# Performance work log

Measured on AMD Instinct MI355X. Metric: run time of the kernel, lower is better.

## Reference

```python
import jax, jax.numpy as jnp
import numpy as np

N, R, E, DIN, DOUT, B = 40000, 16, 50000, 256, 256, 4


def setup_inputs() -> dict:
    key = jax.random.key(0)
    ks = jax.random.split(key, 7)
    xav = (2.0 / (DIN + DOUT)) ** 0.5  # xavier-ish scale
    x = jax.random.normal(ks[0], (N, DIN), jnp.float32)
    bases = jax.random.normal(ks[1], (B, DIN, DOUT), jnp.float32) * xav
    coeff = jax.random.normal(ks[2], (R, B), jnp.float32) * 0.5
    loop_weight = jax.random.normal(ks[3], (DIN, DOUT), jnp.float32) * xav
    h_bias = jnp.zeros((DOUT,), jnp.float32)
    edge_src = jax.random.randint(ks[4], (R, E), 0, N, dtype=jnp.int64)
    edge_dst = jax.random.randint(ks[5], (R, E), 0, N, dtype=jnp.int64)
    return {"x": x, "bases": bases, "coeff": coeff, "loop_weight": loop_weight,
            "h_bias": h_bias, "edge_src": edge_src, "edge_dst": edge_dst}


def reference(x, bases, coeff, loop_weight, h_bias, edge_src, edge_dst):
    # Basis decomposition: per-relation weight W_r = sum_b coeff[r,b] * bases[b]
    W = jnp.einsum('rb,bio->rio', coeff, bases)  # [R, DIN, DOUT]
    n = x.shape[0]

    def body(acc, rel):
        W_r, src, dst = rel
        # transform all nodes once, gather at edge sources
        m = (x @ W_r)[src]                                   # [E, DOUT]
        agg = jax.ops.segment_sum(m, dst, num_segments=n)    # [N, DOUT]
        deg = jax.ops.segment_sum(jnp.ones(src.shape, jnp.float32), dst,
                                  num_segments=n)            # in-degree per rel
        # norm='right': divide by dst in-degree (clamped to 1)
        return acc + agg / jnp.clip(deg, 1.0)[:, None], None

    h0 = jnp.zeros((n, loop_weight.shape[1]), x.dtype)
    h, _ = jax.lax.scan(body, h0, (W, edge_src, edge_dst))   # sum over relations
    h = h + x @ loop_weight + h_bias                         # self-loop + bias
    return jax.nn.relu(h)
```

## Files before the change

kernel.cpp:

```cpp
#include <hip/hip_runtime.h>

#define NN   40000
#define RR   16
#define EE   50000
#define DD   256
#define NB   4
#define KTOT (NB*DD + DD)

#define SCAN_BLK  40
#define SCAN_ELEM 1024

typedef __bf16 bf16x8 __attribute__((ext_vector_type(8)));
typedef float  f32x4  __attribute__((ext_vector_type(4)));
typedef float  f32x2  __attribute__((ext_vector_type(2)));
typedef unsigned short ushort_t;

__device__ inline unsigned short f2bf(float f) {
    unsigned int b = __builtin_bit_cast(unsigned int, f);
    b += 0x7FFFu + ((b >> 16) & 1u);
    return (unsigned short)(b >> 16);
}


__global__ __launch_bounds__(256) void k_cast(const float* __restrict__ x,
                                              const float* __restrict__ bases,
                                              const float* __restrict__ lw,
                                              ushort_t* __restrict__ xb,
                                              ushort_t* __restrict__ Bt) {
    int t = blockIdx.x * blockDim.x + threadIdx.x;
    const int NX = NN * DD / 4;
    if (t < NX) {
        float4 f = *(const float4*)(x + (size_t)t * 4);
        ushort4 o;
        o.x = f2bf(f.x); o.y = f2bf(f.y); o.z = f2bf(f.z); o.w = f2bf(f.w);
        *(ushort4*)(xb + (size_t)t * 4) = o;
    } else {
        int u = t - NX;
        if (u < DD * KTOT) {
            int o = u / KTOT, k = u - o * KTOT;
            float f = (k < NB * DD) ? bases[(size_t)k * DD + o]
                                    : lw[(size_t)(k - NB * DD) * DD + o];
            Bt[u] = f2bf(f);
        }
    }
}

__global__ __launch_bounds__(256) void k_deg(const int* __restrict__ edst,
                                             int* __restrict__ deg) {
    int e = blockIdx.x * blockDim.x + threadIdx.x;
    if (e >= RR * EE) return;
    int r = e / EE;
    atomicAdd(&deg[r * NN + edst[e]], 1);
}

__global__ __launch_bounds__(256) void k_hist(const int* __restrict__ deg,
                                              int* __restrict__ hist) {
    int i = blockIdx.x * blockDim.x + threadIdx.x;
    if (i >= NN) return;
    int s = 0;
#pragma unroll
    for (int r = 0; r < RR; r++) s += deg[r * NN + i];
    hist[i] = s;
}

__global__ __launch_bounds__(256) void k_scanA(const int* __restrict__ hist,
                                               int* __restrict__ offsets,
                                               int* __restrict__ bsum) {
    __shared__ int part[256];
    int t = threadIdx.x, b = blockIdx.x;
    int g = b * SCAN_ELEM + t * 4;
    int4 h = {0, 0, 0, 0};
    if (g + 3 < NN) h = *(const int4*)(hist + g);
    else {
        if (g + 0 < NN) h.x = hist[g + 0];
        if (g + 1 < NN) h.y = hist[g + 1];
        if (g + 2 < NN) h.z = hist[g + 2];
        if (g + 3 < NN) h.w = hist[g + 3];
    }
    int s = h.x + h.y + h.z + h.w;
    part[t] = s;
    __syncthreads();
    for (int off = 1; off < 256; off <<= 1) {
        int v = (t >= off) ? part[t - off] : 0;
        __syncthreads();
        part[t] += v;
        __syncthreads();
    }
    int ex = part[t] - s;
    int4 o;
    o.x = ex;
    o.y = ex + h.x;
    o.z = ex + h.x + h.y;
    o.w = ex + h.x + h.y + h.z;
    if (g + 3 < NN) *(int4*)(offsets + g) = o;
    else {
        if (g + 0 < NN) offsets[g + 0] = o.x;
        if (g + 1 < NN) offsets[g + 1] = o.y;
        if (g + 2 < NN) offsets[g + 2] = o.z;
        if (g + 3 < NN) offsets[g + 3] = o.w;
    }
    if (t == 255) bsum[b] = part[255];
}

__global__ __launch_bounds__(256) void k_scanB(const int* __restrict__ bsum,
                                               int* __restrict__ offsets,
                                               int* __restrict__ cursor) {
    __shared__ int sbase, stot;
    int t = threadIdx.x, b = blockIdx.x;
    if (t == 0) {
        int acc = 0, base = 0;
        for (int i = 0; i < SCAN_BLK; i++) {
            if (i == b) base = acc;
            acc += bsum[i];
        }
        sbase = base;
        stot = acc;
    }
    __syncthreads();
    int base = sbase;
    int g = b * SCAN_ELEM + t * 4;
    if (g + 3 < NN) {
        int4 o = *(const int4*)(offsets + g);
        o.x += base; o.y += base; o.z += base; o.w += base;
        *(int4*)(offsets + g) = o;
        *(int4*)(cursor + g) = o;
    } else {
#pragma unroll
        for (int c = 0; c < 4; c++) {
            if (g + c < NN) {
                int v = offsets[g + c] + base;
                offsets[g + c] = v;
                cursor[g + c] = v;
            }
        }
    }
    if (b == SCAN_BLK - 1 && t == 0) offsets[NN] = stot;
}

__global__ __launch_bounds__(256) void k_escatter(const int* __restrict__ esrc,
                                                  const int* __restrict__ edst,
                                                  int* __restrict__ cursor,
                                                  unsigned int* __restrict__ recs) {
    int e = blockIdx.x * blockDim.x + threadIdx.x;
    if (e >= RR * EE) return;
    int r = e / EE;
    int d = edst[e];
    int pos = atomicAdd(&cursor[d], 1);
    recs[pos] = (unsigned int)esrc[e] | ((unsigned int)r << 16);
}

__global__ __launch_bounds__(256) void k_gather(const ushort_t* __restrict__ xb,
                                                const float* __restrict__ coeff,
                                                const int* __restrict__ deg,
                                                const int* __restrict__ offsets,
                                                const unsigned int* __restrict__ recs,
                                                ushort_t* __restrict__ vb) {
    __shared__ float wtab[4][64];
    int lane = threadIdx.x & 63;
    int wv   = threadIdx.x >> 6;
    int n    = __builtin_amdgcn_readfirstlane(blockIdx.x * 4 + wv);

    {
        int r  = lane >> 2;
        int dg = deg[r * NN + n];
        float inv = 1.0f / (float)(dg > 0 ? dg : 1);
        wtab[wv][lane] = coeff[lane] * inv;
    }

    int beg = offsets[n], end = offsets[n + 1];
    f32x2 a[4][2];
#pragma unroll
    for (int b = 0; b < 4; b++) { a[b][0] = (f32x2){0,0}; a[b][1] = (f32x2){0,0}; }

    const float* wrow = &wtab[wv][0];
    const ushort_t* xl = xb + lane * 4;

    auto acc_edge = [&](uint2 u, float4 w) {
        f32x2 lo, hi;
        lo.x = __builtin_bit_cast(float, u.x << 16);
        lo.y = __builtin_bit_cast(float, u.x & 0xFFFF0000u);
        hi.x = __builtin_bit_cast(float, u.y << 16);
        hi.y = __builtin_bit_cast(float, u.y & 0xFFFF0000u);
        a[0][0] = lo * (f32x2){w.x, w.x} + a[0][0];
        a[0][1] = hi * (f32x2){w.x, w.x} + a[0][1];
        a[1][0] = lo * (f32x2){w.y, w.y} + a[1][0];
        a[1][1] = hi * (f32x2){w.y, w.y} + a[1][1];
        a[2][0] = lo * (f32x2){w.z, w.z} + a[2][0];
        a[2][1] = hi * (f32x2){w.z, w.z} + a[2][1];
        a[3][0] = lo * (f32x2){w.w, w.w} + a[3][0];
        a[3][1] = hi * (f32x2){w.w, w.w} + a[3][1];
    };

    int ei = beg;
    for (; ei + 4 <= end; ei += 4) {
        unsigned int r0 = recs[ei + 0];
        unsigned int r1 = recs[ei + 1];
        unsigned int r2 = recs[ei + 2];
        unsigned int r3 = recs[ei + 3];
        uint2 u0 = *(const uint2*)(xl + (size_t)(r0 & 0xFFFFu) * DD);
        uint2 u1 = *(const uint2*)(xl + (size_t)(r1 & 0xFFFFu) * DD);
        uint2 u2 = *(const uint2*)(xl + (size_t)(r2 & 0xFFFFu) * DD);
        uint2 u3 = *(const uint2*)(xl + (size_t)(r3 & 0xFFFFu) * DD);
        float4 w0 = *(const float4*)&wrow[(r0 >> 16) * 4];
        float4 w1 = *(const float4*)&wrow[(r1 >> 16) * 4];
        float4 w2 = *(const float4*)&wrow[(r2 >> 16) * 4];
        float4 w3 = *(const float4*)&wrow[(r3 >> 16) * 4];
        acc_edge(u0, w0);
        acc_edge(u1, w1);
        acc_edge(u2, w2);
        acc_edge(u3, w3);
    }
    for (; ei < end; ei++) {
        unsigned int r0 = recs[ei];
        uint2 u0 = *(const uint2*)(xl + (size_t)(r0 & 0xFFFFu) * DD);
        float4 w0 = *(const float4*)&wrow[(r0 >> 16) * 4];
        acc_edge(u0, w0);
    }

    ushort_t* vr = vb + (size_t)n * (NB * DD) + lane * 4;
#pragma unroll
    for (int b = 0; b < 4; b++) {
        ushort4 o;
        o.x = f2bf(a[b][0].x); o.y = f2bf(a[b][0].y);
        o.z = f2bf(a[b][1].x); o.w = f2bf(a[b][1].y);
        *(ushort4*)(vr + b * DD) = o;
    }
}

#define LDA 40
__global__ __launch_bounds__(256) void k_gemm(const ushort_t* __restrict__ vb,
                                              const ushort_t* __restrict__ xb,
                                              const ushort_t* __restrict__ Bt,
                                              const float* __restrict__ bias,
                                              float* __restrict__ out) {
    __shared__ ushort_t As[128 * LDA];
    __shared__ ushort_t Bs[128 * LDA];
    int tid  = threadIdx.x;
    int lane = tid & 63;
    int w    = tid >> 6;
    int wr   = w >> 1, wc = w & 1;
    int rowbase = blockIdx.x * 128;
    int nbase   = blockIdx.y * 128;

    f32x4 acc[4][4];
#pragma unroll
    for (int i = 0; i < 4; i++)
#pragma unroll
        for (int j = 0; j < 4; j++) acc[i][j] = (f32x4){0,0,0,0};

    int m0 = wr * 64 + (lane & 15);
    int n0 = wc * 64 + (lane & 15);
    int kq = (lane >> 4) * 8;

    for (int kb = 0; kb < KTOT; kb += 32) {
        __syncthreads();
#pragma unroll
        for (int s = 0; s < 2; s++) {
            int e = s * 256 + tid;
            int row = e >> 2, ch = (e & 3) * 8;
            int node = min(rowbase + row, NN - 1);
            const ushort_t* asrc = (kb < NB * DD)
                ? vb + (size_t)node * (NB * DD) + kb + ch
                : xb + (size_t)node * DD + (kb - NB * DD) + ch;
            uint4 av = *(const uint4*)asrc;
            const ushort_t* bsrc = Bt + (size_t)(nbase + row) * KTOT + kb + ch;
            uint4 bv = *(const uint4*)bsrc;
            *(uint4*)&As[row * LDA + ch] = av;
            *(uint4*)&Bs[row * LDA + ch] = bv;
        }
        __syncthreads();

        bf16x8 af[4], bf[4];
#pragma unroll
        for (int i = 0; i < 4; i++)
            af[i] = *(const bf16x8*)&As[(m0 + i * 16) * LDA + kq];
#pragma unroll
        for (int j = 0; j < 4; j++)
            bf[j] = *(const bf16x8*)&Bs[(n0 + j * 16) * LDA + kq];
#pragma unroll
        for (int i = 0; i < 4; i++)
#pragma unroll
            for (int j = 0; j < 4; j++)
                acc[i][j] = __builtin_amdgcn_mfma_f32_16x16x32_bf16(af[i], bf[j], acc[i][j], 0, 0, 0);
    }

#pragma unroll
    for (int i = 0; i < 4; i++) {
#pragma unroll
        for (int r = 0; r < 4; r++) {
            int row = wr * 64 + i * 16 + (lane >> 4) * 4 + r;
            int ng = rowbase + row;
            if (ng >= NN) continue;
#pragma unroll
            for (int j = 0; j < 4; j++) {
                int o = nbase + wc * 64 + j * 16 + (lane & 15);
                float vv = acc[i][j][r] + bias[o];
                out[(size_t)ng * DD + o] = fmaxf(vv, 0.0f);
            }
        }
    }
}

extern "C" void kernel_launch(void* const* d_in, const int* in_sizes, int n_in,
                              void* d_out, int out_size, void* d_ws, size_t ws_size,
                              hipStream_t stream) {
    const float* x     = (const float*)d_in[0];
    const float* bases = (const float*)d_in[1];
    const float* coeff = (const float*)d_in[2];
    const float* lw    = (const float*)d_in[3];
    const float* bias  = (const float*)d_in[4];
    const int*   esrc  = (const int*)d_in[5];
    const int*   edst  = (const int*)d_in[6];
    float* out = (float*)d_out;

    char* ws = (char*)d_ws;
    ushort_t*     vb      = (ushort_t*)(ws);
    ushort_t*     xb      = (ushort_t*)(ws + 81920000);
    ushort_t*     Bt      = (ushort_t*)(ws + 102400000);
    int*          deg     = (int*)(ws + 103055360);
    int*          hist    = (int*)(ws + 105615360);
    int*          offsets = (int*)(ws + 105775360);
    int*          cursor  = (int*)(ws + 105935376);
    unsigned int* recs    = (unsigned int*)(ws + 106095376);
    int*          bsum    = (int*)(ws + 109295376);

    hipMemsetAsync(deg, 0, (size_t)RR * NN * sizeof(int), stream);

    int ne = RR * EE;
    int ncast = NN * DD / 4 + DD * KTOT;
    k_cast<<<(ncast + 255) / 256, 256, 0, stream>>>(x, bases, lw, xb, Bt);
    k_deg<<<(ne + 255) / 256, 256, 0, stream>>>(edst, deg);
    k_hist<<<(NN + 255) / 256, 256, 0, stream>>>(deg, hist);
    k_scanA<<<SCAN_BLK, 256, 0, stream>>>(hist, offsets, bsum);
    k_scanB<<<SCAN_BLK, 256, 0, stream>>>(bsum, offsets, cursor);
    k_escatter<<<(ne + 255) / 256, 256, 0, stream>>>(esrc, edst, cursor, recs);
    k_gather<<<NN / 4, 256, 0, stream>>>(xb, coeff, deg, offsets, recs, vb);
    dim3 ggrid((NN + 127) / 128, 2);
    k_gemm<<<ggrid, 256, 0, stream>>>(vb, xb, Bt, bias, out);
}
```

Measured before the change: 320.3 us.

## Restructure GEMM with direct-to-LDS A loads, register-held B, and fuse hist into scan

The GEMM now stages only the A tile in LDS, using global_load_lds with an XOR-swizzled layout and a K step of 64. B fragments load straight from global into registers, and each wave computes a 32x128 strip. Bias is hoisted into registers and the kernel requests 3 blocks per SM. The separate histogram kernel is folded into scanA, which sums the 16 per-relation degree rows directly, removing one launch and an intermediate buffer. The B loads are no longer shared through LDS, so each wave rereads B from global or cache, which raises register pressure and cache traffic.

```diff
diff --git a/kernel.cpp b/kernel.cpp
--- a/kernel.cpp
+++ b/kernel.cpp
@@ -19,6 +19,13 @@
     unsigned int b = __builtin_bit_cast(unsigned int, f);
     b += 0x7FFFu + ((b >> 16) & 1u);
     return (unsigned short)(b >> 16);
+}
+
+__device__ __forceinline__ void load_lds16(const ushort_t* g, ushort_t* l) {
+    __builtin_amdgcn_global_load_lds(
+        (const __attribute__((address_space(1))) unsigned int*)g,
+        (__attribute__((address_space(3))) unsigned int*)l,
+        16, 0, 0);
 }
 
 
@@ -53,29 +60,19 @@
     atomicAdd(&deg[r * NN + edst[e]], 1);
 }
 
-__global__ __launch_bounds__(256) void k_hist(const int* __restrict__ deg,
-                                              int* __restrict__ hist) {
-    int i = blockIdx.x * blockDim.x + threadIdx.x;
-    if (i >= NN) return;
-    int s = 0;
-#pragma unroll
-    for (int r = 0; r < RR; r++) s += deg[r * NN + i];
-    hist[i] = s;
-}
-
-__global__ __launch_bounds__(256) void k_scanA(const int* __restrict__ hist,
+__global__ __launch_bounds__(256) void k_scanA(const int* __restrict__ deg,
                                                int* __restrict__ offsets,
                                                int* __restrict__ bsum) {
     __shared__ int part[256];
     int t = threadIdx.x, b = blockIdx.x;
     int g = b * SCAN_ELEM + t * 4;
     int4 h = {0, 0, 0, 0};
-    if (g + 3 < NN) h = *(const int4*)(hist + g);
-    else {
-        if (g + 0 < NN) h.x = hist[g + 0];
-        if (g + 1 < NN) h.y = hist[g + 1];
-        if (g + 2 < NN) h.z = hist[g + 2];
-        if (g + 3 < NN) h.w = hist[g + 3];
+    if (g < NN) {
+#pragma unroll
+        for (int r = 0; r < RR; r++) {
+            int4 d = *(const int4*)(deg + (size_t)r * NN + g);
+            h.x += d.x; h.y += d.y; h.z += d.z; h.w += d.w;
+        }
     }
     int s = h.x + h.y + h.z + h.w;
     part[t] = s;
@@ -87,17 +84,13 @@
         __syncthreads();
     }
     int ex = part[t] - s;
-    int4 o;
-    o.x = ex;
-    o.y = ex + h.x;
-    o.z = ex + h.x + h.y;
-    o.w = ex + h.x + h.y + h.z;
-    if (g + 3 < NN) *(int4*)(offsets + g) = o;
-    else {
-        if (g + 0 < NN) offsets[g + 0] = o.x;
-        if (g + 1 < NN) offsets[g + 1] = o.y;
-        if (g + 2 < NN) offsets[g + 2] = o.z;
-        if (g + 3 < NN) offsets[g + 3] = o.w;
+    if (g < NN) {
+        int4 o;
+        o.x = ex;
+        o.y = ex + h.x;
+        o.z = ex + h.x + h.y;
+        o.w = ex + h.x + h.y + h.z;
+        *(int4*)(offsets + g) = o;
     }
     if (t == 255) bsum[b] = part[255];
 }
@@ -119,20 +112,11 @@
     __syncthreads();
     int base = sbase;
     int g = b * SCAN_ELEM + t * 4;
-    if (g + 3 < NN) {
+    if (g < NN) {
         int4 o = *(const int4*)(offsets + g);
         o.x += base; o.y += base; o.z += base; o.w += base;
         *(int4*)(offsets + g) = o;
         *(int4*)(cursor + g) = o;
-    } else {
-#pragma unroll
-        for (int c = 0; c < 4; c++) {
-            if (g + c < NN) {
-                int v = offsets[g + c] + base;
-                offsets[g + c] = v;
-                cursor[g + c] = v;
-            }
-        }
     }
     if (b == SCAN_BLK - 1 && t == 0) offsets[NN] = stot;
 }
@@ -227,75 +211,85 @@
     }
 }
 
-#define LDA 40
-__global__ __launch_bounds__(256) void k_gemm(const ushort_t* __restrict__ vb,
-                                              const ushort_t* __restrict__ xb,
-                                              const ushort_t* __restrict__ Bt,
-                                              const float* __restrict__ bias,
-                                              float* __restrict__ out) {
-    __shared__ ushort_t As[128 * LDA];
-    __shared__ ushort_t Bs[128 * LDA];
+__global__ __launch_bounds__(256, 3) void k_gemm(const ushort_t* __restrict__ vb,
+                                                 const ushort_t* __restrict__ xb,
+                                                 const ushort_t* __restrict__ Bt,
+                                                 const float* __restrict__ bias,
+                                                 float* __restrict__ out) {
+    __shared__ ushort_t As[128 * 64];
     int tid  = threadIdx.x;
     int lane = tid & 63;
     int w    = tid >> 6;
-    int wr   = w >> 1, wc = w & 1;
     int rowbase = blockIdx.x * 128;
     int nbase   = blockIdx.y * 128;
 
-    f32x4 acc[4][4];
-#pragma unroll
-    for (int i = 0; i < 4; i++)
-#pragma unroll
-        for (int j = 0; j < 4; j++) acc[i][j] = (f32x4){0,0,0,0};
-
-    int m0 = wr * 64 + (lane & 15);
-    int n0 = wc * 64 + (lane & 15);
-    int kq = (lane >> 4) * 8;
-
-    for (int kb = 0; kb < KTOT; kb += 32) {
+    int q  = lane >> 4;
+    int ml = lane & 15;
+    int srow   = lane >> 3;
+    int schunk = (lane & 7) ^ srow;
+
+    f32x4 acc[2][8];
+#pragma unroll
+    for (int i = 0; i < 2; i++)
+#pragma unroll
+        for (int j = 0; j < 8; j++) acc[i][j] = (f32x4){0,0,0,0};
+
+    float bv[8];
+#pragma unroll
+    for (int j = 0; j < 8; j++) bv[j] = bias[nbase + j * 16 + ml];
+
+    const ushort_t* bp = Bt + (size_t)(nbase + ml) * KTOT + q * 8;
+
+    for (int kb = 0; kb < KTOT; kb += 64) {
+        bf16x8 bfr[2][8];
+#pragma unroll
+        for (int ks = 0; ks < 2; ks++)
+#pragma unroll
+            for (int j = 0; j < 8; j++)
+                bfr[ks][j] = *(const bf16x8*)(bp + (size_t)j * 16 * KTOT + kb + ks * 32);
+
         __syncthreads();
 #pragma unroll
-        for (int s = 0; s < 2; s++) {
-            int e = s * 256 + tid;
-            int row = e >> 2, ch = (e & 3) * 8;
-            int node = min(rowbase + row, NN - 1);
-            const ushort_t* asrc = (kb < NB * DD)
-                ? vb + (size_t)node * (NB * DD) + kb + ch
-                : xb + (size_t)node * DD + (kb - NB * DD) + ch;
-            uint4 av = *(const uint4*)asrc;
-            const ushort_t* bsrc = Bt + (size_t)(nbase + row) * KTOT + kb + ch;
-            uint4 bv = *(const uint4*)bsrc;
-            *(uint4*)&As[row * LDA + ch] = av;
-            *(uint4*)&Bs[row * LDA + ch] = bv;
+        for (int s = 0; s < 4; s++) {
+            int grp = w * 4 + s;
+            int rl  = grp * 8 + srow;
+            int node = rowbase + rl;
+            if (node > NN - 1) node = NN - 1;
+            const ushort_t* g = (kb < NB * DD)
+                ? vb + (size_t)node * (NB * DD) + kb + schunk * 8
+                : xb + (size_t)node * DD + (kb - NB * DD) + schunk * 8;
+            load_lds16(g, &As[grp * 64 * 8]);
         }
         __syncthreads();
 
-        bf16x8 af[4], bf[4];
-#pragma unroll
-        for (int i = 0; i < 4; i++)
-            af[i] = *(const bf16x8*)&As[(m0 + i * 16) * LDA + kq];
-#pragma unroll
-        for (int j = 0; j < 4; j++)
-            bf[j] = *(const bf16x8*)&Bs[(n0 + j * 16) * LDA + kq];
-#pragma unroll
-        for (int i = 0; i < 4; i++)
-#pragma unroll
-            for (int j = 0; j < 4; j++)
-                acc[i][j] = __builtin_amdgcn_mfma_f32_16x16x32_bf16(af[i], bf[j], acc[i][j], 0, 0, 0);
-    }
-
-#pragma unroll
-    for (int i = 0; i < 4; i++) {
+#pragma unroll
+        for (int ks = 0; ks < 2; ks++) {
+            bf16x8 af[2];
+#pragma unroll
+            for (int i = 0; i < 2; i++) {
+                int m = w * 32 + i * 16 + ml;
+                int a16 = m * 8 + ((ks * 4 + q) ^ (m & 7));
+                af[i] = *(const bf16x8*)&As[a16 * 8];
+            }
+#pragma unroll
+            for (int i = 0; i < 2; i++)
+#pragma unroll
+                for (int j = 0; j < 8; j++)
+                    acc[i][j] = __builtin_amdgcn_mfma_f32_16x16x32_bf16(af[i], bfr[ks][j], acc[i][j], 0, 0, 0);
+        }
+    }
+
+#pragma unroll
+    for (int i = 0; i < 2; i++) {
 #pragma unroll
         for (int r = 0; r < 4; r++) {
-            int row = wr * 64 + i * 16 + (lane >> 4) * 4 + r;
-            int ng = rowbase + row;
+            int rl = w * 32 + i * 16 + q * 4 + r;
+            int ng = rowbase + rl;
             if (ng >= NN) continue;
 #pragma unroll
-            for (int j = 0; j < 4; j++) {
-                int o = nbase + wc * 64 + j * 16 + (lane & 15);
-                float vv = acc[i][j][r] + bias[o];
-                out[(size_t)ng * DD + o] = fmaxf(vv, 0.0f);
+            for (int j = 0; j < 8; j++) {
+                float vvv = acc[i][j][r] + bv[j];
+                out[(size_t)ng * DD + nbase + j * 16 + ml] = fmaxf(vvv, 0.0f);
             }
         }
     }
@@ -318,7 +312,6 @@
     ushort_t*     xb      = (ushort_t*)(ws + 81920000);
     ushort_t*     Bt      = (ushort_t*)(ws + 102400000);
     int*          deg     = (int*)(ws + 103055360);
-    int*          hist    = (int*)(ws + 105615360);
     int*          offsets = (int*)(ws + 105775360);
     int*          cursor  = (int*)(ws + 105935376);
     unsigned int* recs    = (unsigned int*)(ws + 106095376);
@@ -330,8 +323,7 @@
     int ncast = NN * DD / 4 + DD * KTOT;
     k_cast<<<(ncast + 255) / 256, 256, 0, stream>>>(x, bases, lw, xb, Bt);
     k_deg<<<(ne + 255) / 256, 256, 0, stream>>>(edst, deg);
-    k_hist<<<(NN + 255) / 256, 256, 0, stream>>>(deg, hist);
-    k_scanA<<<SCAN_BLK, 256, 0, stream>>>(hist, offsets, bsum);
+    k_scanA<<<SCAN_BLK, 256, 0, stream>>>(deg, offsets, bsum);
     k_scanB<<<SCAN_BLK, 256, 0, stream>>>(bsum, offsets, cursor);
     k_escatter<<<(ne + 255) / 256, 256, 0, stream>>>(esrc, edst, cursor, recs);
     k_gather<<<NN / 4, 256, 0, stream>>>(xb, coeff, deg, offsets, recs, vb);
```

Result: slower. 368.6 us (+15.1%).
